# Performance work log

Hardware: AMD Instinct MI355X
Metric: run time of the kernel (lower is better)

## Reference

```python
import jax, jax.numpy as jnp
import numpy as np

N = 4096; B = 4; NPB = N // B; K = 16
C = 128; COUT = 128; LMAX = 2; L = (LMAX + 1) ** 2  # 9 SH coefficients
H = 8; A = 8; V = 16; HV = H * V
F = 256; NB = 128; FD = 256; CUTOFF = 3.0
E = N * K

def _silu(x):
    return x * jax.nn.sigmoid(x)

def _mish(x):
    return x * jnp.tanh(jax.nn.softplus(x))

def _rms_norm(x, gamma):
    # degree-wise RMS over channel dim, x: [N, L, C]
    s = jnp.sqrt(jnp.mean(x * x, axis=-1, keepdims=True) + 1e-6)
    return x / s * gamma

def _rot_l1(x, R):
    # rotate the l=1 block (coeffs 1:4) of x [E, L, C] by R [E, 3, 3]
    l1 = jnp.einsum('eij,ejc->eic', R, x[:, 1:4, :])
    return jnp.concatenate([x[:, :1, :], l1, x[:, 4:, :]], axis=1)

def _knn(coord, batch):
    d2 = jnp.sum((coord[:, None, :] - coord[None, :, :]) ** 2, axis=-1)  # [N,N]
    same = batch[:, None] == batch[None, :]
    big = jnp.asarray(1e9, d2.dtype)
    d2 = jnp.where(same, d2, big)
    d2 = d2.at[jnp.arange(N), jnp.arange(N)].set(big)
    neg, idx = jax.lax.top_k(-d2, K)
    dist = jnp.sqrt(jnp.maximum(-neg, 0.0))
    edge_src = idx.reshape(-1)                       # [E]
    edge_dst = jnp.repeat(jnp.arange(N), K)          # [E]
    valid = (dist <= CUTOFF).reshape(-1)
    return edge_src, edge_dst, valid

def _edge_rot_mat(edge_vec):
    # deterministic rotation aligning each edge with the y-axis (eSCN-style)
    nx = edge_vec / (jnp.linalg.norm(edge_vec, axis=-1, keepdims=True) + 1e-12)
    ref = jnp.where(jnp.abs(nx[:, :1]) < 0.9,
                    jnp.array([1.0, 0.0, 0.0], nx.dtype),
                    jnp.array([0.0, 1.0, 0.0], nx.dtype))
    nz = jnp.cross(nx, ref)
    nz = nz / (jnp.linalg.norm(nz, axis=-1, keepdims=True) + 1e-12)
    ny = jnp.cross(nz, nx)
    return jnp.stack([nz, nx, ny], axis=1)  # [E,3,3]; R @ edge_dir = e_y

def _forward(node_coord, node_emb, batch, condition,
             W_e1, b_e1, W_e2, b_e2, W_src, W_dst, w_a, W_v, W_o,
             gamma1, gamma2, W_g, W_f1, W_f2, W_film, b_film):
    # dynamic KNN graph; geometry detached as in original (edge_vec.detach())
    coord_g = jax.lax.stop_gradient(node_coord)
    edge_src, edge_dst, valid = _knn(coord_g, batch)
    edge_vec = coord_g[edge_src] - coord_g[edge_dst]                  # [E,3]
    edge_len = jnp.linalg.norm(edge_vec, axis=-1)                     # [E]
    R = _edge_rot_mat(edge_vec)                                       # [E,3,3]
    # gaussian radial basis -> per-edge embedding
    mu = jnp.linspace(0.0, CUTOFF, NB)
    sigma = CUTOFF / NB
    rbf = jnp.exp(-0.5 * ((edge_len[:, None] - mu) / sigma) ** 2)     # [E,NB]
    edge_h = _silu(rbf @ W_e1 + b_e1) @ W_e2 + b_e2                   # [E,HV]
    # equivariant attention (rotate into edge frame, attend, rotate back)
    x_src = _rot_l1(node_emb[edge_src], R)                            # [E,L,C]
    q = node_emb[edge_dst, 0] @ W_dst + x_src[:, 0] @ W_src           # [E,H*A]
    logits = jnp.einsum('eha,ha->eh', _silu(q).reshape(E, H, A), w_a)
    logits = jnp.where(valid[:, None], logits, -1e9)
    m = jax.ops.segment_max(logits, edge_dst, num_segments=N)
    ex = jnp.exp(logits - m[edge_dst])
    den = jax.ops.segment_sum(ex, edge_dst, num_segments=N)
    attn = ex / (den[edge_dst] + 1e-9)                                # [E,H]
    v = jnp.einsum('elc,cv->elv', x_src, W_v) * edge_h[:, None, :]    # [E,L,HV]
    v = v.reshape(E, L, H, V) * attn[:, None, :, None]
    msg = _rot_l1(v.reshape(E, L, HV), jnp.swapaxes(R, 1, 2))         # back to global frame
    agg = jax.ops.segment_sum(msg, edge_dst, num_segments=N)          # [N,L,HV]
    x = node_emb + jnp.einsum('nlv,vc->nlc', agg, W_o)
    # FFN with separable S2 (scalar-gated) activation
    h = _rms_norm(x, gamma2)
    gate = _silu(h[:, 0] @ W_g)                                       # [N,F]
    hid = jnp.einsum('nlc,cf->nlf', h, W_f1) * gate[:, None, :]
    x = x + jnp.einsum('nlf,fo->nlo', hid, W_f2)
    x = _rms_norm(x, gamma1)
    # FiLM conditioning over flattened (L*C) per batch element
    film = _mish(condition) @ W_film + b_film                         # [B, 2*L*COUT]
    w, bfi = film[:, :L * COUT], film[:, L * COUT:]
    c = x.reshape(B, NPB, L * COUT) * w[:, None, :] + bfi[:, None, :]
    return c.reshape(N, L, COUT)

def setup_inputs():
    key = jax.random.key(0)
    ks = jax.random.split(key, 16)
    node_coord = jax.random.uniform(ks[0], (N, 3)) * 2.0
    node_emb = jax.random.normal(ks[1], (N, L, C)) * 0.1
    batch = jnp.arange(N, dtype=jnp.int64 if jax.config.jax_enable_x64 else jnp.int32) // NPB
    condition = jax.random.normal(ks[2], (B, FD))
    s = lambda d: 1.0 / np.sqrt(d)
    return {
        'node_coord': node_coord, 'node_emb': node_emb, 'batch': batch, 'condition': condition,
        'W_e1': jax.random.normal(ks[3], (NB, 128)) * s(NB), 'b_e1': jnp.zeros((128,)),
        'W_e2': jax.random.normal(ks[4], (128, HV)) * s(128), 'b_e2': jnp.zeros((HV,)),
        'W_src': jax.random.normal(ks[5], (C, H * A)) * s(C),
        'W_dst': jax.random.normal(ks[6], (C, H * A)) * s(C),
        'w_a': jax.random.normal(ks[7], (H, A)) * s(A),
        'W_v': jax.random.normal(ks[8], (C, HV)) * s(C),
        'W_o': jax.random.normal(ks[9], (HV, C)) * s(HV),
        'gamma1': jnp.ones((C,)), 'gamma2': jnp.ones((C,)),
        'W_g': jax.random.normal(ks[10], (C, F)) * s(C),
        'W_f1': jax.random.normal(ks[11], (C, F)) * s(C),
        'W_f2': jax.random.normal(ks[12], (F, COUT)) * s(F),
        'W_film': jax.random.normal(ks[13], (FD, 2 * L * COUT)) * s(FD),
        'b_film': jnp.zeros((2 * L * COUT,)),
    }

def reference(node_coord, node_emb, batch, condition,
              W_e1, b_e1, W_e2, b_e2, W_src, W_dst, w_a, W_v, W_o,
              gamma1, gamma2, W_g, W_f1, W_f2, W_film, b_film):
    out = _forward(node_coord, node_emb, batch, condition,
                   W_e1, b_e1, W_e2, b_e2, W_src, W_dst, w_a, W_v, W_o,
                   gamma1, gamma2, W_g, W_f1, W_f2, W_film, b_film)
    return (node_coord, out, batch)
```

## Files before the change

### kernel.cpp

```cpp
#include <hip/hip_runtime.h>

#define NNODE 4096
#define NPB   1024

__device__ __forceinline__ float siluf(float x){ return x / (1.0f + expf(-x)); }

__global__ __launch_bounds__(256) void k_film(const float* __restrict__ cond,
                                              const float* __restrict__ Wfilm,
                                              const float* __restrict__ bfilm,
                                              float* __restrict__ filmG){
  __shared__ float mL[256];
  int b = blockIdx.y;
  int t = threadIdx.x;
  int j = blockIdx.x*256 + t;
  float x = cond[b*256 + t];
  float sp = fmaxf(x, 0.f) + log1pf(expf(-fabsf(x)));
  mL[t] = x * tanhf(sp);
  __syncthreads();
  if(j >= 2304) return;
  float acc = bfilm[j];
  for(int i=0;i<256;i++) acc += mL[i] * Wfilm[i*2304 + j];
  filmG[b*2304 + j] = acc;
}

__global__ __launch_bounds__(256) void k_pre(const float* __restrict__ emb,
                                             const float* __restrict__ Wv,
                                             const float* __restrict__ Wsrc,
                                             const float* __restrict__ Wdst,
                                             float* __restrict__ ZG,
                                             float* __restrict__ QsG,
                                             float* __restrict__ QdG){
  const int t = threadIdx.x;
  const int rg = __builtin_amdgcn_readfirstlane(t >> 6);
  const int lane = t & 63;
  const int c0 = lane*2;
  const int n = blockIdx.x*4 + rg;
  const float* en = emb + (size_t)n*1152;

  float z[9][2];
  #pragma unroll
  for(int l=0;l<9;l++){ z[l][0]=0.f; z[l][1]=0.f; }
  for(int c4=0;c4<32;c4++){
    float2 wv0 = *(const float2*)&Wv[(c4*4+0)*128 + c0];
    float2 wv1 = *(const float2*)&Wv[(c4*4+1)*128 + c0];
    float2 wv2 = *(const float2*)&Wv[(c4*4+2)*128 + c0];
    float2 wv3 = *(const float2*)&Wv[(c4*4+3)*128 + c0];
    #pragma unroll
    for(int l=0;l<9;l++){
      float4 x4 = *(const float4*)&en[l*128 + c4*4];
      z[l][0] += x4.x*wv0.x + x4.y*wv1.x + x4.z*wv2.x + x4.w*wv3.x;
      z[l][1] += x4.x*wv0.y + x4.y*wv1.y + x4.z*wv2.y + x4.w*wv3.y;
    }
  }
  #pragma unroll
  for(int l=0;l<9;l++){
    float2 o; o.x=z[l][0]; o.y=z[l][1];
    *(float2*)&ZG[(size_t)n*1152 + l*128 + c0] = o;
  }
  float qs = 0.f, qd = 0.f;
  for(int c=0;c<128;c++){
    float ec = en[c];
    qs = fmaf(ec, Wsrc[c*64 + lane], qs);
    qd = fmaf(ec, Wdst[c*64 + lane], qd);
  }
  QsG[n*64 + lane] = qs;
  QdG[n*64 + lane] = qd;
}

#define E2_HD   0
#define E2_RB   2048
#define E2_AT   2304
#define E2_KI   2432
#define E2_LEN  2448
#define E2_VL   2464
#define E2_W0   2480
#define F_ACT   0
#define F_HID   1152
#define E2_NPF  2560
__global__ __launch_bounds__(128, 4) void k_node(
    const float* __restrict__ coord,
    const float* __restrict__ emb,
    const float* __restrict__ We1, const float* __restrict__ be1,
    const float* __restrict__ We2, const float* __restrict__ be2,
    const float* __restrict__ wa,
    const float* __restrict__ Wo,
    const float* __restrict__ g1, const float* __restrict__ g2,
    const float* __restrict__ Wg, const float* __restrict__ Wf1,
    const float* __restrict__ Wf2,
    const float* __restrict__ Qs, const float* __restrict__ Qd,
    const float* __restrict__ Z,
    const float* __restrict__ filmG,
    float* __restrict__ out){
  __shared__ __align__(16) float S[2*E2_NPF];
  int* Si = (int*)S;
  const int t = threadIdx.x;
  const int w = __builtin_amdgcn_readfirstlane(t >> 6);
  const int lane = t & 63;
  const int n = blockIdx.x*2 + w;
  const int base = n & ~(NPB - 1);
  const int self = n - base;
  const int NP = w * E2_NPF;
  const int c0 = lane*2;
  const int myh = lane >> 3;

  {
    const float* cb = coord + (size_t)base*3;
    const float cx = cb[self*3+0];
    const float cy = cb[self*3+1];
    const float cz = cb[self*3+2];
    float d2a[16]; int ida[16];
    #pragma unroll
    for(int q=0;q<16;q++){
      int j = lane + q*64;
      float dx = __fsub_rn(cb[j*3+0], cx);
      float dy = __fsub_rn(cb[j*3+1], cy);
      float dz = __fsub_rn(cb[j*3+2], cz);
      float d2 = __fadd_rn(__fadd_rn(__fmul_rn(dx,dx), __fmul_rn(dy,dy)), __fmul_rn(dz,dz));
      if(j == self) d2 = 3e38f;
      d2a[q] = d2; ida[q] = j;
    }
    #pragma unroll 1
    for(int r=0;r<16;r++){
      float bd = d2a[0]; int bi = ida[0];
      #pragma unroll
      for(int q=1;q<16;q++){
        bool bet = (d2a[q] < bd) || (d2a[q] == bd && ida[q] < bi);
        if(bet){ bd = d2a[q]; bi = ida[q]; }
      }
      #pragma unroll
      for(int s=1;s<64;s<<=1){
        float od = __shfl_xor(bd, s, 64);
        int   oi = __shfl_xor(bi, s, 64);
        bool bet = (od < bd) || (od == bd && oi < bi);
        if(bet){ bd = od; bi = oi; }
      }
      if(lane == 0){
        Si[NP + E2_KI + r] = bi;
        float len = __fsqrt_rn(bd);
        S[NP + E2_LEN + r] = len;
        S[NP + E2_VL + r]  = (len <= 3.0f) ? 1.0f : 0.0f;
        int i0 = (int)(len * (127.0f/3.0f) + 0.5f);
        int w0 = i0 - 7;
        w0 = w0 < 0 ? 0 : (w0 > 112 ? 112 : w0);
        Si[NP + E2_W0 + r] = w0;
      }
      #pragma unroll
      for(int q=0;q<16;q++) if(ida[q] == bi) d2a[q] = 3e38f;
    }
  }
  __syncthreads();

  {
    const int e0 = lane >> 3, hh = lane & 7;
    float4 qda = *(const float4*)&Qd[(size_t)n*64 + hh*8];
    float4 qdb = *(const float4*)&Qd[(size_t)n*64 + hh*8 + 4];
    float4 waa = *(const float4*)&wa[hh*8];
    float4 wab = *(const float4*)&wa[hh*8 + 4];
    float lg[2];
    #pragma unroll
    for(int s=0;s<2;s++){
      int e = e0 + s*8;
      int src = base + Si[NP + E2_KI + e];
      float4 qa = *(const float4*)&Qs[(size_t)src*64 + hh*8];
      float4 qb = *(const float4*)&Qs[(size_t)src*64 + hh*8 + 4];
      float sv = siluf(qda.x+qa.x)*waa.x + siluf(qda.y+qa.y)*waa.y
               + siluf(qda.z+qa.z)*waa.z + siluf(qda.w+qa.w)*waa.w
               + siluf(qdb.x+qb.x)*wab.x + siluf(qdb.y+qb.y)*wab.y
               + siluf(qdb.z+qb.z)*wab.z + siluf(qdb.w+qb.w)*wab.w;
      lg[s] = (S[NP + E2_VL + e] > 0.5f) ? sv : -1e9f;
    }
    float m = fmaxf(lg[0], lg[1]);
    m = fmaxf(m, __shfl_xor(m, 8, 64));
    m = fmaxf(m, __shfl_xor(m, 16, 64));
    m = fmaxf(m, __shfl_xor(m, 32, 64));
    float ex0 = expf(lg[0] - m), ex1 = expf(lg[1] - m);
    float den = ex0 + ex1;
    den += __shfl_xor(den, 8, 64);
    den += __shfl_xor(den, 16, 64);
    den += __shfl_xor(den, 32, 64);
    float inv = 1.0f/(den + 1e-9f);
    S[NP + E2_AT + lane]      = ex0*inv;
    S[NP + E2_AT + 64 + lane] = ex1*inv;

    const float step = 3.0f/127.0f;
    const float sigma = 3.0f/128.0f;
    #pragma unroll
    for(int k=0;k<4;k++){
      int idx = lane + k*64;
      int e = idx >> 4, wi = idx & 15;
      float len = S[NP + E2_LEN + e];
      int bin = Si[NP + E2_W0 + e] + wi;
      float d = (len - step*(float)bin) / sigma;
      S[NP + E2_RB + idx] = expf(-0.5f*d*d);
    }
  }
  __syncthreads();

  {
    float a4[16][2]; int b0e[16];
    #pragma unroll
    for(int e=0;e<16;e++){ a4[e][0]=0.f; a4[e][1]=0.f; b0e[e] = Si[NP + E2_W0 + e]; }
    #pragma unroll 1
    for(int wi=0; wi<16; wi++){
      #pragma unroll
      for(int e=0;e<16;e++){
        float rb = S[NP + E2_RB + e*16 + wi];
        float2 we = *(const float2*)&We1[(size_t)(b0e[e] + wi)*128 + c0];
        a4[e][0] = fmaf(rb, we.x, a4[e][0]);
        a4[e][1] = fmaf(rb, we.y, a4[e][1]);
      }
    }
    float2 b1v = *(const float2*)&be1[c0];
    #pragma unroll
    for(int e=0;e<16;e++){
      float2 o; o.x = siluf(a4[e][0] + b1v.x); o.y = siluf(a4[e][1] + b1v.y);
      *(float2*)&S[NP + E2_HD + e*128 + c0] = o;
    }
  }
  __syncthreads();

  float a5[16][2];
  #pragma unroll
  for(int e=0;e<16;e++){ a5[e][0]=0.f; a5[e][1]=0.f; }
  #pragma unroll 1
  for(int c4=0;c4<32;c4++){
    float2 w0 = *(const float2*)&We2[(c4*4+0)*128 + c0];
    float2 w1 = *(const float2*)&We2[(c4*4+1)*128 + c0];
    float2 w2 = *(const float2*)&We2[(c4*4+2)*128 + c0];
    float2 w3 = *(const float2*)&We2[(c4*4+3)*128 + c0];
    #pragma unroll
    for(int e=0;e<16;e++){
      float4 h4 = *(const float4*)&S[NP + E2_HD + e*128 + c4*4];
      a5[e][0] += h4.x*w0.x + h4.y*w1.x + h4.z*w2.x + h4.w*w3.x;
      a5[e][1] += h4.x*w0.y + h4.y*w1.y + h4.z*w2.y + h4.w*w3.y;
    }
  }

  {
    float2 b2v = *(const float2*)&be2[c0];
    float ag[9][2];
    #pragma unroll
    for(int l=0;l<9;l++){ ag[l][0]=0.f; ag[l][1]=0.f; }
    #pragma unroll 4
    for(int e=0;e<16;e++){
      int src = base + Si[NP + E2_KI + e];
      const float* zp = &Z[(size_t)src*1152 + c0];
      float at = S[NP + E2_AT + e*8 + myh];
      float sc0 = (a5[e][0] + b2v.x) * at;
      float sc1 = (a5[e][1] + b2v.y) * at;
      #pragma unroll
      for(int l=0;l<9;l++){
        float2 z2 = *(const float2*)&zp[l*128];
        ag[l][0] = fmaf(z2.x, sc0, ag[l][0]);
        ag[l][1] = fmaf(z2.y, sc1, ag[l][1]);
      }
    }
    #pragma unroll
    for(int l=0;l<9;l++){
      float2 o; o.x = ag[l][0]; o.y = ag[l][1];
      *(float2*)&S[NP + F_ACT + l*128 + c0] = o;
    }
  }

  float* W_ = &S[NP];

  float x[9][2];
  #pragma unroll
  for(int l=0;l<9;l++){ x[l][0]=0.f; x[l][1]=0.f; }
  #pragma unroll 1
  for(int c4=0;c4<32;c4++){
    float2 w0 = *(const float2*)&Wo[(c4*4+0)*128 + c0];
    float2 w1 = *(const float2*)&Wo[(c4*4+1)*128 + c0];
    float2 w2 = *(const float2*)&Wo[(c4*4+2)*128 + c0];
    float2 w3 = *(const float2*)&Wo[(c4*4+3)*128 + c0];
    #pragma unroll
    for(int l=0;l<9;l++){
      float4 a4 = *(const float4*)&W_[F_ACT + l*128 + c4*4];
      x[l][0] += a4.x*w0.x + a4.y*w1.x + a4.z*w2.x + a4.w*w3.x;
      x[l][1] += a4.x*w0.y + a4.y*w1.y + a4.z*w2.y + a4.w*w3.y;
    }
  }

  {
    float g2a = g2[c0], g2b = g2[c0+1];
    #pragma unroll
    for(int l=0;l<9;l++){
      float2 e2 = *(const float2*)&emb[(size_t)n*1152 + l*128 + c0];
      x[l][0] += e2.x; x[l][1] += e2.y;
      float sq = x[l][0]*x[l][0] + x[l][1]*x[l][1];
      #pragma unroll
      for(int s=1;s<64;s<<=1) sq += __shfl_xor(sq, s, 64);
      float ss = sqrtf(sq/128.f + 1e-6f);
      float2 o; o.x = x[l][0]/ss*g2a; o.y = x[l][1]/ss*g2b;
      *(float2*)&W_[F_ACT + l*128 + c0] = o;
    }
  }

  #pragma unroll 1
  for(int ft=0;ft<2;ft++){
    float ha[9][2]; float ga0 = 0.f, ga1 = 0.f;
    #pragma unroll
    for(int l=0;l<9;l++){ ha[l][0]=0.f; ha[l][1]=0.f; }
    #pragma unroll 1
    for(int c4=0;c4<32;c4++){
      float2 wf0 = *(const float2*)&Wf1[(c4*4+0)*256 + ft*128 + c0];
      float2 wf1 = *(const float2*)&Wf1[(c4*4+1)*256 + ft*128 + c0];
      float2 wf2 = *(const float2*)&Wf1[(c4*4+2)*256 + ft*128 + c0];
      float2 wf3 = *(const float2*)&Wf1[(c4*4+3)*256 + ft*128 + c0];
      float2 wg0 = *(const float2*)&Wg [(c4*4+0)*256 + ft*128 + c0];
      float2 wg1 = *(const float2*)&Wg [(c4*4+1)*256 + ft*128 + c0];
      float2 wg2 = *(const float2*)&Wg [(c4*4+2)*256 + ft*128 + c0];
      float2 wg3 = *(const float2*)&Wg [(c4*4+3)*256 + ft*128 + c0];
      float4 h0 = *(const float4*)&W_[F_ACT + 0*128 + c4*4];
      ga0 += h0.x*wg0.x + h0.y*wg1.x + h0.z*wg2.x + h0.w*wg3.x;
      ga1 += h0.x*wg0.y + h0.y*wg1.y + h0.z*wg2.y + h0.w*wg3.y;
      ha[0][0] += h0.x*wf0.x + h0.y*wf1.x + h0.z*wf2.x + h0.w*wf3.x;
      ha[0][1] += h0.x*wf0.y + h0.y*wf1.y + h0.z*wf2.y + h0.w*wf3.y;
      #pragma unroll
      for(int l=1;l<9;l++){
        float4 h4 = *(const float4*)&W_[F_ACT + l*128 + c4*4];
        ha[l][0] += h4.x*wf0.x + h4.y*wf1.x + h4.z*wf2.x + h4.w*wf3.x;
        ha[l][1] += h4.x*wf0.y + h4.y*wf1.y + h4.z*wf2.y + h4.w*wf3.y;
      }
    }
    float gx = siluf(ga0), gy = siluf(ga1);
    #pragma unroll
    for(int l=0;l<9;l++){
      float2 o; o.x = ha[l][0]*gx; o.y = ha[l][1]*gy;
      *(float2*)&W_[F_HID + l*128 + c0] = o;
    }
    #pragma unroll 1
    for(int f4=0;f4<32;f4++){
      float2 w0 = *(const float2*)&Wf2[(ft*128 + f4*4+0)*128 + c0];
      float2 w1 = *(const float2*)&Wf2[(ft*128 + f4*4+1)*128 + c0];
      float2 w2 = *(const float2*)&Wf2[(ft*128 + f4*4+2)*128 + c0];
      float2 w3 = *(const float2*)&Wf2[(ft*128 + f4*4+3)*128 + c0];
      #pragma unroll
      for(int l=0;l<9;l++){
        float4 h4 = *(const float4*)&W_[F_HID + l*128 + f4*4];
        x[l][0] += h4.x*w0.x + h4.y*w1.x + h4.z*w2.x + h4.w*w3.x;
        x[l][1] += h4.x*w0.y + h4.y*w1.y + h4.z*w2.y + h4.w*w3.y;
      }
    }
  }

  {
    float g1a = g1[c0], g1b = g1[c0+1];
    int b = n >> 10;
    #pragma unroll
    for(int l=0;l<9;l++){
      float sq = x[l][0]*x[l][0] + x[l][1]*x[l][1];
      #pragma unroll
      for(int s=1;s<64;s<<=1) sq += __shfl_xor(sq, s, 64);
      float ss = sqrtf(sq/128.f + 1e-6f);
      float2 fw = *(const float2*)&filmG[b*2304 + l*128 + c0];
      float2 fb = *(const float2*)&filmG[b*2304 + 1152 + l*128 + c0];
      float2 o;
      o.x = x[l][0]/ss*g1a*fw.x + fb.x;
      o.y = x[l][1]/ss*g1b*fw.y + fb.y;
      *(float2*)&out[12288 + (size_t)n*1152 + l*128 + c0] = o;
    }
  }
}

__global__ __launch_bounds__(256) void k_copy(const float* __restrict__ coord,
                                              float* __restrict__ out){
  int i = blockIdx.x*256 + threadIdx.x;
  if(i < 12288) out[i] = coord[i];
  int n = i - 12288;
  if(n >= 0 && n < 4096) out[12288 + 4718592 + n] = (float)(n >> 10);
}

extern "C" void kernel_launch(void* const* d_in, const int* in_sizes, int n_in,
                              void* d_out, int out_size, void* d_ws, size_t ws_size,
                              hipStream_t stream) {
  const float* coord = (const float*)d_in[0];
  const float* emb   = (const float*)d_in[1];
  const float* cond  = (const float*)d_in[3];
  const float* We1   = (const float*)d_in[4];
  const float* be1   = (const float*)d_in[5];
  const float* We2   = (const float*)d_in[6];
  const float* be2   = (const float*)d_in[7];
  const float* Wsrc  = (const float*)d_in[8];
  const float* Wdst  = (const float*)d_in[9];
  const float* wa    = (const float*)d_in[10];
  const float* Wv    = (const float*)d_in[11];
  const float* Wo    = (const float*)d_in[12];
  const float* g1    = (const float*)d_in[13];
  const float* g2    = (const float*)d_in[14];
  const float* Wg    = (const float*)d_in[15];
  const float* Wf1   = (const float*)d_in[16];
  const float* Wf2   = (const float*)d_in[17];
  const float* Wfilm = (const float*)d_in[18];
  const float* bfilm = (const float*)d_in[19];

  float* outf  = (float*)d_out;
  float* filmG = (float*)d_ws;
  float* QsG   = filmG + 9216;
  float* QdG   = QsG + 262144;
  float* ZG    = QdG + 262144;

  k_film<<<dim3(9,4), 256, 0, stream>>>(cond, Wfilm, bfilm, filmG);
  k_pre<<<NNODE/4, 256, 0, stream>>>(emb, Wv, Wsrc, Wdst, ZG, QsG, QdG);
  k_node<<<NNODE/2, 128, 0, stream>>>(coord, emb,
                                      We1, be1, We2, be2, wa,
                                      Wo, g1, g2, Wg, Wf1, Wf2,
                                      QsG, QdG, ZG, filmG, outf);
  k_copy<<<64, 256, 0, stream>>>(coord, outf);
}
```

Measured before the change: 400.0 us.

## Use packed FP32 FMA inline asm for matvecs and swizzle block-to-node mapping

```diff
diff --git a/kernel.cpp b/kernel.cpp
--- a/kernel.cpp
+++ b/kernel.cpp
@@ -3,7 +3,28 @@
 #define NNODE 4096
 #define NPB   1024
 
+typedef float v2f __attribute__((ext_vector_type(2)));
+typedef float v4f __attribute__((ext_vector_type(4)));
+
 __device__ __forceinline__ float siluf(float x){ return x / (1.0f + expf(-x)); }
+
+__device__ __forceinline__ v2f pk_fma_lo(v2f a, v2f b, v2f c){
+  v2f d;
+  asm("v_pk_fma_f32 %0, %1, %2, %3 op_sel_hi:[1,0,1]" : "=v"(d) : "v"(a), "v"(b), "v"(c));
+  return d;
+}
+__device__ __forceinline__ v2f pk_fma_hi(v2f a, v2f b, v2f c){
+  v2f d;
+  asm("v_pk_fma_f32 %0, %1, %2, %3 op_sel:[0,1,0] op_sel_hi:[1,1,1]" : "=v"(d) : "v"(a), "v"(b), "v"(c));
+  return d;
+}
+__device__ __forceinline__ v2f pk_fma2(v2f a, v2f b, v2f c){
+  v2f d;
+  asm("v_pk_fma_f32 %0, %1, %2, %3" : "=v"(d) : "v"(a), "v"(b), "v"(c));
+  return d;
+}
+#define SHLO(h) __builtin_shufflevector((h), (h), 0, 1)
+#define SHHI(h) __builtin_shufflevector((h), (h), 2, 3)
 
 __global__ __launch_bounds__(256) void k_film(const float* __restrict__ cond,
                                               const float* __restrict__ Wfilm,
@@ -37,26 +58,26 @@
   const int n = blockIdx.x*4 + rg;
   const float* en = emb + (size_t)n*1152;
 
-  float z[9][2];
+  v2f z[9];
   #pragma unroll
-  for(int l=0;l<9;l++){ z[l][0]=0.f; z[l][1]=0.f; }
+  for(int l=0;l<9;l++) z[l] = (v2f)0.0f;
   for(int c4=0;c4<32;c4++){
-    float2 wv0 = *(const float2*)&Wv[(c4*4+0)*128 + c0];
-    float2 wv1 = *(const float2*)&Wv[(c4*4+1)*128 + c0];
-    float2 wv2 = *(const float2*)&Wv[(c4*4+2)*128 + c0];
-    float2 wv3 = *(const float2*)&Wv[(c4*4+3)*128 + c0];
+    v2f wv0 = *(const v2f*)&Wv[(c4*4+0)*128 + c0];
+    v2f wv1 = *(const v2f*)&Wv[(c4*4+1)*128 + c0];
+    v2f wv2 = *(const v2f*)&Wv[(c4*4+2)*128 + c0];
+    v2f wv3 = *(const v2f*)&Wv[(c4*4+3)*128 + c0];
     #pragma unroll
     for(int l=0;l<9;l++){
-      float4 x4 = *(const float4*)&en[l*128 + c4*4];
-      z[l][0] += x4.x*wv0.x + x4.y*wv1.x + x4.z*wv2.x + x4.w*wv3.x;
-      z[l][1] += x4.x*wv0.y + x4.y*wv1.y + x4.z*wv2.y + x4.w*wv3.y;
+      v4f x4 = *(const v4f*)&en[l*128 + c4*4];
+      v2f h01 = SHLO(x4), h23 = SHHI(x4);
+      z[l] = pk_fma_lo(wv0, h01, z[l]);
+      z[l] = pk_fma_hi(wv1, h01, z[l]);
+      z[l] = pk_fma_lo(wv2, h23, z[l]);
+      z[l] = pk_fma_hi(wv3, h23, z[l]);
     }
   }
   #pragma unroll
-  for(int l=0;l<9;l++){
-    float2 o; o.x=z[l][0]; o.y=z[l][1];
-    *(float2*)&ZG[(size_t)n*1152 + l*128 + c0] = o;
-  }
+  for(int l=0;l<9;l++) *(v2f*)&ZG[(size_t)n*1152 + l*128 + c0] = z[l];
   float qs = 0.f, qd = 0.f;
   for(int c=0;c<128;c++){
     float ec = en[c];
@@ -96,7 +117,9 @@
   const int t = threadIdx.x;
   const int w = __builtin_amdgcn_readfirstlane(t >> 6);
   const int lane = t & 63;
-  const int n = blockIdx.x*2 + w;
+  const int bid = blockIdx.x;
+  const int sbid = (bid & 7) * (NNODE/16) + (bid >> 3);
+  const int n = sbid*2 + w;
   const int base = n & ~(NPB - 1);
   const int self = n - base;
   const int NP = w * E2_NPF;
@@ -219,65 +242,66 @@
   }
   __syncthreads();
 
-  float a5[16][2];
+  v2f a5[16];
   #pragma unroll
-  for(int e=0;e<16;e++){ a5[e][0]=0.f; a5[e][1]=0.f; }
+  for(int e=0;e<16;e++) a5[e] = (v2f)0.0f;
   #pragma unroll 1
   for(int c4=0;c4<32;c4++){
-    float2 w0 = *(const float2*)&We2[(c4*4+0)*128 + c0];
-    float2 w1 = *(const float2*)&We2[(c4*4+1)*128 + c0];
-    float2 w2 = *(const float2*)&We2[(c4*4+2)*128 + c0];
-    float2 w3 = *(const float2*)&We2[(c4*4+3)*128 + c0];
+    v2f w0 = *(const v2f*)&We2[(c4*4+0)*128 + c0];
+    v2f w1 = *(const v2f*)&We2[(c4*4+1)*128 + c0];
+    v2f w2 = *(const v2f*)&We2[(c4*4+2)*128 + c0];
+    v2f w3 = *(const v2f*)&We2[(c4*4+3)*128 + c0];
     #pragma unroll
     for(int e=0;e<16;e++){
-      float4 h4 = *(const float4*)&S[NP + E2_HD + e*128 + c4*4];
-      a5[e][0] += h4.x*w0.x + h4.y*w1.x + h4.z*w2.x + h4.w*w3.x;
-      a5[e][1] += h4.x*w0.y + h4.y*w1.y + h4.z*w2.y + h4.w*w3.y;
-    }
-  }
-
-  {
-    float2 b2v = *(const float2*)&be2[c0];
-    float ag[9][2];
-    #pragma unroll
-    for(int l=0;l<9;l++){ ag[l][0]=0.f; ag[l][1]=0.f; }
+      v4f h4 = *(const v4f*)&S[NP + E2_HD + e*128 + c4*4];
+      v2f h01 = SHLO(h4), h23 = SHHI(h4);
+      a5[e] = pk_fma_lo(w0, h01, a5[e]);
+      a5[e] = pk_fma_hi(w1, h01, a5[e]);
+      a5[e] = pk_fma_lo(w2, h23, a5[e]);
+      a5[e] = pk_fma_hi(w3, h23, a5[e]);
+    }
+  }
+
+  {
+    v2f b2v = *(const v2f*)&be2[c0];
+    v2f ag[9];
+    #pragma unroll
+    for(int l=0;l<9;l++) ag[l] = (v2f)0.0f;
     #pragma unroll 4
     for(int e=0;e<16;e++){
       int src = base + Si[NP + E2_KI + e];
       const float* zp = &Z[(size_t)src*1152 + c0];
       float at = S[NP + E2_AT + e*8 + myh];
-      float sc0 = (a5[e][0] + b2v.x) * at;
-      float sc1 = (a5[e][1] + b2v.y) * at;
+      v2f sc = (a5[e] + b2v) * at;
       #pragma unroll
       for(int l=0;l<9;l++){
-        float2 z2 = *(const float2*)&zp[l*128];
-        ag[l][0] = fmaf(z2.x, sc0, ag[l][0]);
-        ag[l][1] = fmaf(z2.y, sc1, ag[l][1]);
-      }
-    }
-    #pragma unroll
-    for(int l=0;l<9;l++){
-      float2 o; o.x = ag[l][0]; o.y = ag[l][1];
-      *(float2*)&S[NP + F_ACT + l*128 + c0] = o;
-    }
+        v2f z2 = *(const v2f*)&zp[l*128];
+        ag[l] = pk_fma2(z2, sc, ag[l]);
+      }
+    }
+    #pragma unroll
+    for(int l=0;l<9;l++) *(v2f*)&S[NP + F_ACT + l*128 + c0] = ag[l];
   }
 
   float* W_ = &S[NP];
 
-  float x[9][2];
+  v2f x[9];
   #pragma unroll
-  for(int l=0;l<9;l++){ x[l][0]=0.f; x[l][1]=0.f; }
+  for(int l=0;l<9;l++) x[l] = (v2f)0.0f;
   #pragma unroll 1
   for(int c4=0;c4<32;c4++){
-    float2 w0 = *(const float2*)&Wo[(c4*4+0)*128 + c0];
-    float2 w1 = *(const float2*)&Wo[(c4*4+1)*128 + c0];
-    float2 w2 = *(const float2*)&Wo[(c4*4+2)*128 + c0];
-    float2 w3 = *(const float2*)&Wo[(c4*4+3)*128 + c0];
+    v2f w0 = *(const v2f*)&Wo[(c4*4+0)*128 + c0];
+    v2f w1 = *(const v2f*)&Wo[(c4*4+1)*128 + c0];
+    v2f w2 = *(const v2f*)&Wo[(c4*4+2)*128 + c0];
+    v2f w3 = *(const v2f*)&Wo[(c4*4+3)*128 + c0];
     #pragma unroll
     for(int l=0;l<9;l++){
-      float4 a4 = *(const float4*)&W_[F_ACT + l*128 + c4*4];
-      x[l][0] += a4.x*w0.x + a4.y*w1.x + a4.z*w2.x + a4.w*w3.x;
-      x[l][1] += a4.x*w0.y + a4.y*w1.y + a4.z*w2.y + a4.w*w3.y;
+      v4f a4 = *(const v4f*)&W_[F_ACT + l*128 + c4*4];
+      v2f h01 = SHLO(a4), h23 = SHHI(a4);
+      x[l] = pk_fma_lo(w0, h01, x[l]);
+      x[l] = pk_fma_hi(w1, h01, x[l]);
+      x[l] = pk_fma_lo(w2, h23, x[l]);
+      x[l] = pk_fma_hi(w3, h23, x[l]);
     }
   }
 
@@ -285,61 +309,72 @@
     float g2a = g2[c0], g2b = g2[c0+1];
     #pragma unroll
     for(int l=0;l<9;l++){
-      float2 e2 = *(const float2*)&emb[(size_t)n*1152 + l*128 + c0];
-      x[l][0] += e2.x; x[l][1] += e2.y;
+      v2f e2 = *(const v2f*)&emb[(size_t)n*1152 + l*128 + c0];
+      x[l] += e2;
       float sq = x[l][0]*x[l][0] + x[l][1]*x[l][1];
       #pragma unroll
       for(int s=1;s<64;s<<=1) sq += __shfl_xor(sq, s, 64);
       float ss = sqrtf(sq/128.f + 1e-6f);
-      float2 o; o.x = x[l][0]/ss*g2a; o.y = x[l][1]/ss*g2b;
-      *(float2*)&W_[F_ACT + l*128 + c0] = o;
+      v2f o; o.x = x[l][0]/ss*g2a; o.y = x[l][1]/ss*g2b;
+      *(v2f*)&W_[F_ACT + l*128 + c0] = o;
     }
   }
 
   #pragma unroll 1
   for(int ft=0;ft<2;ft++){
-    float ha[9][2]; float ga0 = 0.f, ga1 = 0.f;
-    #pragma unroll
-    for(int l=0;l<9;l++){ ha[l][0]=0.f; ha[l][1]=0.f; }
+    v2f ha[9]; v2f ga = (v2f)0.0f;
+    #pragma unroll
+    for(int l=0;l<9;l++) ha[l] = (v2f)0.0f;
     #pragma unroll 1
     for(int c4=0;c4<32;c4++){
-      float2 wf0 = *(const float2*)&Wf1[(c4*4+0)*256 + ft*128 + c0];
-      float2 wf1 = *(const float2*)&Wf1[(c4*4+1)*256 + ft*128 + c0];
-      float2 wf2 = *(const float2*)&Wf1[(c4*4+2)*256 + ft*128 + c0];
-      float2 wf3 = *(const float2*)&Wf1[(c4*4+3)*256 + ft*128 + c0];
-      float2 wg0 = *(const float2*)&Wg [(c4*4+0)*256 + ft*128 + c0];
-      float2 wg1 = *(const float2*)&Wg [(c4*4+1)*256 + ft*128 + c0];
-      float2 wg2 = *(const float2*)&Wg [(c4*4+2)*256 + ft*128 + c0];
-      float2 wg3 = *(const float2*)&Wg [(c4*4+3)*256 + ft*128 + c0];
-      float4 h0 = *(const float4*)&W_[F_ACT + 0*128 + c4*4];
-      ga0 += h0.x*wg0.x + h0.y*wg1.x + h0.z*wg2.x + h0.w*wg3.x;
-      ga1 += h0.x*wg0.y + h0.y*wg1.y + h0.z*wg2.y + h0.w*wg3.y;
-      ha[0][0] += h0.x*wf0.x + h0.y*wf1.x + h0.z*wf2.x + h0.w*wf3.x;
-      ha[0][1] += h0.x*wf0.y + h0.y*wf1.y + h0.z*wf2.y + h0.w*wf3.y;
+      v2f wf0 = *(const v2f*)&Wf1[(c4*4+0)*256 + ft*128 + c0];
+      v2f wf1 = *(const v2f*)&Wf1[(c4*4+1)*256 + ft*128 + c0];
+      v2f wf2 = *(const v2f*)&Wf1[(c4*4+2)*256 + ft*128 + c0];
+      v2f wf3 = *(const v2f*)&Wf1[(c4*4+3)*256 + ft*128 + c0];
+      v2f wg0 = *(const v2f*)&Wg [(c4*4+0)*256 + ft*128 + c0];
+      v2f wg1 = *(const v2f*)&Wg [(c4*4+1)*256 + ft*128 + c0];
+      v2f wg2 = *(const v2f*)&Wg [(c4*4+2)*256 + ft*128 + c0];
+      v2f wg3 = *(const v2f*)&Wg [(c4*4+3)*256 + ft*128 + c0];
+      v4f h0 = *(const v4f*)&W_[F_ACT + 0*128 + c4*4];
+      v2f h01 = SHLO(h0), h23 = SHHI(h0);
+      ga = pk_fma_lo(wg0, h01, ga);
+      ga = pk_fma_hi(wg1, h01, ga);
+      ga = pk_fma_lo(wg2, h23, ga);
+      ga = pk_fma_hi(wg3, h23, ga);
+      ha[0] = pk_fma_lo(wf0, h01, ha[0]);
+      ha[0] = pk_fma_hi(wf1, h01, ha[0]);
+      ha[0] = pk_fma_lo(wf2, h23, ha[0]);
+      ha[0] = pk_fma_hi(wf3, h23, ha[0]);
       #pragma unroll
       for(int l=1;l<9;l++){
-        float4 h4 = *(const float4*)&W_[F_ACT + l*128 + c4*4];
-        ha[l][0] += h4.x*wf0.x + h4.y*wf1.x + h4.z*wf2.x + h4.w*wf3.x;
-        ha[l][1] += h4.x*wf0.y + h4.y*wf1.y + h4.z*wf2.y + h4.w*wf3.y;
-      }
-    }
-    float gx = siluf(ga0), gy = siluf(ga1);
+        v4f h4 = *(const v4f*)&W_[F_ACT + l*128 + c4*4];
+        v2f a01 = SHLO(h4), a23 = SHHI(h4);
+        ha[l] = pk_fma_lo(wf0, a01, ha[l]);
+        ha[l] = pk_fma_hi(wf1, a01, ha[l]);
+        ha[l] = pk_fma_lo(wf2, a23, ha[l]);
+        ha[l] = pk_fma_hi(wf3, a23, ha[l]);
+      }
+    }
+    float gx = siluf(ga[0]), gy = siluf(ga[1]);
     #pragma unroll
     for(int l=0;l<9;l++){
-      float2 o; o.x = ha[l][0]*gx; o.y = ha[l][1]*gy;
-      *(float2*)&W_[F_HID + l*128 + c0] = o;
+      v2f o; o.x = ha[l][0]*gx; o.y = ha[l][1]*gy;
+      *(v2f*)&W_[F_HID + l*128 + c0] = o;
     }
     #pragma unroll 1
     for(int f4=0;f4<32;f4++){
-      float2 w0 = *(const float2*)&Wf2[(ft*128 + f4*4+0)*128 + c0];
-      float2 w1 = *(const float2*)&Wf2[(ft*128 + f4*4+1)*128 + c0];
-      float2 w2 = *(const float2*)&Wf2[(ft*128 + f4*4+2)*128 + c0];
-      float2 w3 = *(const float2*)&Wf2[(ft*128 + f4*4+3)*128 + c0];
+      v2f w0 = *(const v2f*)&Wf2[(ft*128 + f4*4+0)*128 + c0];
+      v2f w1 = *(const v2f*)&Wf2[(ft*128 + f4*4+1)*128 + c0];
+      v2f w2 = *(const v2f*)&Wf2[(ft*128 + f4*4+2)*128 + c0];
+      v2f w3 = *(const v2f*)&Wf2[(ft*128 + f4*4+3)*128 + c0];
       #pragma unroll
       for(int l=0;l<9;l++){
-        float4 h4 = *(const float4*)&W_[F_HID + l*128 + f4*4];
-        x[l][0] += h4.x*w0.x + h4.y*w1.x + h4.z*w2.x + h4.w*w3.x;
-        x[l][1] += h4.x*w0.y + h4.y*w1.y + h4.z*w2.y + h4.w*w3.y;
+        v4f h4 = *(const v4f*)&W_[F_HID + l*128 + f4*4];
+        v2f h01 = SHLO(h4), h23 = SHHI(h4);
+        x[l] = pk_fma_lo(w0, h01, x[l]);
+        x[l] = pk_fma_hi(w1, h01, x[l]);
+        x[l] = pk_fma_lo(w2, h23, x[l]);
+        x[l] = pk_fma_hi(w3, h23, x[l]);
       }
     }
   }
@@ -353,12 +388,12 @@
       #pragma unroll
       for(int s=1;s<64;s<<=1) sq += __shfl_xor(sq, s, 64);
       float ss = sqrtf(sq/128.f + 1e-6f);
-      float2 fw = *(const float2*)&filmG[b*2304 + l*128 + c0];
-      float2 fb = *(const float2*)&filmG[b*2304 + 1152 + l*128 + c0];
-      float2 o;
+      v2f fw = *(const v2f*)&filmG[b*2304 + l*128 + c0];
+      v2f fb = *(const v2f*)&filmG[b*2304 + 1152 + l*128 + c0];
+      v2f o;
       o.x = x[l][0]/ss*g1a*fw.x + fb.x;
       o.y = x[l][1]/ss*g1b*fw.y + fb.y;
-      *(float2*)&out[12288 + (size_t)n*1152 + l*128 + c0] = o;
+      *(v2f*)&out[12288 + (size_t)n*1152 + l*128 + c0] = o;
     }
   }
 }
```

Result: faster. 368.9 us (-7.8%).
